# Kernel tuning notes

Hardware: AMD Instinct MI355X
Metric: run time of the kernel (lower is better)

## Reference

```python
import jax, jax.numpy as jnp
import numpy as np

C = 1024
H = 16
HS = C // H
HID = 4096
A_MIX = 0.7
B_MIX = 0.3
EPS = 1e-5


def layernorm(x, w, b):
    mu = jnp.mean(x, axis=-1, keepdims=True)
    var = jnp.mean(jnp.square(x - mu), axis=-1, keepdims=True)
    return (x - mu) * jax.lax.rsqrt(var + EPS) * w + b


def setup_inputs() -> dict:
    key = jax.random.key(0)
    ks = jax.random.split(key, 12)
    B, N = 4, 1024
    s = 1.0 / np.sqrt(C)
    sh = 1.0 / np.sqrt(HID)
    return {
        "x": jax.random.normal(ks[0], (B, N, C), jnp.float32),
        "Query": jax.random.normal(ks[1], (B, H, N, HS), jnp.float32),
        "Key": jax.random.normal(ks[2], (B, H, N, HS), jnp.float32),
        "Value": jax.random.normal(ks[3], (B, H, N, HS), jnp.float32),
        "ln_w": jnp.ones((C,), jnp.float32),
        "ln_b": jnp.zeros((C,), jnp.float32),
        "qk_w": jax.random.normal(ks[4], (2 * C, C), jnp.float32) * s,
        "qk_b": jnp.zeros((2 * C,), jnp.float32),
        "v_w": jax.random.normal(ks[5], (C, C), jnp.float32) * s,
        "v_b": jnp.zeros((C,), jnp.float32),
        "out_w": jax.random.normal(ks[6], (C, C), jnp.float32) * s,
        "out_b": jnp.zeros((C,), jnp.float32),
        "mlp_w1": jax.random.normal(ks[7], (HID, C), jnp.float32) * s,
        "mlp_b1": jnp.zeros((HID,), jnp.float32),
        "mlp_w2": jax.random.normal(ks[8], (C, HID), jnp.float32) * sh,
        "mlp_b2": jnp.zeros((C,), jnp.float32),
    }


def reference(x, Query, Key, Value, ln_w, ln_b, qk_w, qk_b, v_w, v_b,
              out_w, out_b, mlp_w1, mlp_b1, mlp_w2, mlp_b2):
    B, N, _ = x.shape
    x1 = x
    xn = layernorm(x, ln_w, ln_b)
    # qk projection -> view (B,N,H,HS,2), permute -> (2,B,H,N,HS)
    qk = (xn @ qk_w.T + qk_b).reshape(B, N, H, HS, 2)
    Q = jnp.transpose(qk[..., 0], (0, 2, 1, 3))  # (B,H,N,HS)
    K = jnp.transpose(qk[..., 1], (0, 2, 1, 3))
    V = jnp.transpose((xn @ v_w.T + v_b).reshape(B, N, H, HS), (0, 2, 1, 3))
    Query = A_MIX * Q + B_MIX * Query
    Key = A_MIX * K + B_MIX * Key
    Value = B_MIX * Value + A_MIX * V
    attn = jnp.einsum('bhqd,bhkd->bhqk', Query, Key) / np.sqrt(HS)
    attn = jax.nn.softmax(attn, axis=-1)  # dropout = identity in eval
    o = jnp.einsum('bhqk,bhkd->bhqd', attn, Value)
    o = jnp.transpose(o, (0, 2, 1, 3)).reshape(B, N, C)
    o = o @ out_w.T + out_b
    x = x1 + o
    x2 = x
    xn2 = layernorm(x, ln_w, ln_b)  # same layernorm params reused
    h = jax.nn.gelu(xn2 @ mlp_w1.T + mlp_b1, approximate=False)
    m = h @ mlp_w2.T + mlp_b2
    return (m + x2, Query, Key, Value)
```

## Files before the change

### kernel.cpp

```cpp
#include <hip/hip_runtime.h>

using bf16x8 = __attribute__((ext_vector_type(8))) __bf16;
using f32x4  = __attribute__((ext_vector_type(4))) float;

#define AS1(p) (const __attribute__((address_space(1))) void*)(p)
#define AS3(p) (__attribute__((address_space(3))) void*)(p)

__device__ __forceinline__ unsigned short f2bf(float f) {
    unsigned int u = __float_as_uint(f);
    unsigned int r = (u + 0x7FFFu + ((u >> 16) & 1u)) >> 16;
    return (unsigned short)r;
}
__device__ __forceinline__ float bf2f(unsigned short u) {
    return __uint_as_float((unsigned int)u << 16);
}
__device__ __forceinline__ float gelu_fast(float x) {
    const float a = 1.5957691f * (x + 0.044715f * x * x * x);
    return x / (1.0f + __expf(-a));
}

__global__ __launch_bounds__(256) void cvt_kernel(const float* __restrict__ in,
                                                  unsigned short* __restrict__ out,
                                                  int n) {
    int i = (blockIdx.x * 256 + threadIdx.x) * 4;
    if (i < n) {
        float4 v = *(const float4*)(in + i);
        ushort4 o = make_ushort4(f2bf(v.x), f2bf(v.y), f2bf(v.z), f2bf(v.w));
        *(ushort4*)(out + i) = o;
    }
}

__global__ __launch_bounds__(256) void ln_kernel(const float* __restrict__ in,
                                                 const float* __restrict__ w,
                                                 const float* __restrict__ b,
                                                 unsigned short* __restrict__ out) {
    const int row = blockIdx.x;
    const int tid = threadIdx.x;
    const float4 v = *(const float4*)(in + (size_t)row * 1024 + tid * 4);
    float s  = v.x + v.y + v.z + v.w;
    float ss = v.x * v.x + v.y * v.y + v.z * v.z + v.w * v.w;
    #pragma unroll
    for (int m = 1; m < 64; m <<= 1) {
        s  += __shfl_xor(s, m, 64);
        ss += __shfl_xor(ss, m, 64);
    }
    __shared__ float red[8];
    if ((tid & 63) == 0) { red[(tid >> 6) * 2] = s; red[(tid >> 6) * 2 + 1] = ss; }
    __syncthreads();
    s  = red[0] + red[2] + red[4] + red[6];
    ss = red[1] + red[3] + red[5] + red[7];
    const float mu  = s * (1.0f / 1024.0f);
    const float var = ss * (1.0f / 1024.0f) - mu * mu;
    const float rstd = rsqrtf(var + 1e-5f);
    const float4 wv = *(const float4*)(w + tid * 4);
    const float4 bv = *(const float4*)(b + tid * 4);
    ushort4 o;
    o.x = f2bf((v.x - mu) * rstd * wv.x + bv.x);
    o.y = f2bf((v.y - mu) * rstd * wv.y + bv.y);
    o.z = f2bf((v.z - mu) * rstd * wv.z + bv.z);
    o.w = f2bf((v.w - mu) * rstd * wv.w + bv.w);
    *(ushort4*)(out + (size_t)row * 1024 + tid * 4) = o;
}

template <int EPI>
__global__ __launch_bounds__(256, 2)
void gemm_bt(const unsigned short* __restrict__ A,
             const unsigned short* __restrict__ W,
             const float* __restrict__ bias,
             int M, int N, int K,
             const float* __restrict__ e0, const float* __restrict__ e1,
             float* __restrict__ o0, float* __restrict__ o1,
             unsigned short* __restrict__ u0, unsigned short* __restrict__ u1) {
    __shared__ unsigned short As[128 * 128];
    __shared__ unsigned short Bs[128 * 128];
    const int tid  = threadIdx.x;
    const int wave = tid >> 6, lane = tid & 63;
    const int wr = wave >> 1, wc = wave & 1;
    const int q15 = lane & 15, g = lane >> 4;

    const int gx = gridDim.x;
    const int nwg = gx * gridDim.y;
    int flat = blockIdx.y * gx + blockIdx.x;
    flat = (flat & 7) * (nwg >> 3) + (flat >> 3);
    const int gm0 = (flat / gx) * 128, gn0 = (flat % gx) * 128;

    f32x4 acc[4][4] = {};

    const int lrow4 = lane >> 4;
    const int lslot = lane & 15;
    const int rswz  = q15 << 4;

    for (int k0 = 0; k0 < K; k0 += 128) {
        #pragma unroll
        for (int i = 0; i < 8; ++i) {
            const int row  = wave * 32 + i * 4 + lrow4;
            const int selm = (lslot ^ (row & 15)) << 3;
            __builtin_amdgcn_global_load_lds(AS1(A + (size_t)(gm0 + row) * K + k0 + selm),
                                             AS3((char*)As + wave * 8192 + i * 1024), 16, 0, 0);
            __builtin_amdgcn_global_load_lds(AS1(W + (size_t)(gn0 + row) * K + k0 + selm),
                                             AS3((char*)Bs + wave * 8192 + i * 1024), 16, 0, 0);
        }
        __syncthreads();
        #pragma unroll
        for (int kk = 0; kk < 4; ++kk) {
            bf16x8 af[4], bfr[4];
            #pragma unroll
            for (int m = 0; m < 4; ++m)
                af[m] = *(const bf16x8*)((char*)As + (wr * 64 + m * 16 + q15) * 256 +
                                         ((kk * 64 + g * 16) ^ rswz));
            #pragma unroll
            for (int n = 0; n < 4; ++n)
                bfr[n] = *(const bf16x8*)((char*)Bs + (wc * 64 + n * 16 + q15) * 256 +
                                          ((kk * 64 + g * 16) ^ rswz));
            #pragma unroll
            for (int m = 0; m < 4; ++m)
                #pragma unroll
                for (int n = 0; n < 4; ++n)
                    acc[m][n] = __builtin_amdgcn_mfma_f32_16x16x32_bf16(af[m], bfr[n], acc[m][n], 0, 0, 0);
        }
        __syncthreads();
    }

    #pragma unroll
    for (int m = 0; m < 4; ++m)
    #pragma unroll
    for (int n = 0; n < 4; ++n)
    #pragma unroll
    for (int j = 0; j < 4; ++j) {
        const int r = gm0 + wr * 64 + m * 16 + g * 4 + j;
        const int c = gn0 + wc * 64 + n * 16 + q15;
        const float val = acc[m][n][j] + bias[c];
        if constexpr (EPI == 0) {
            const int bb = r >> 10, nn = r & 1023;
            const int h = c >> 7, hs = (c >> 1) & 63, isk = c & 1;
            const size_t idx = (((size_t)(bb * 16 + h)) * 1024 + nn) * 64 + hs;
            if (!isk) { const float mx = 0.7f * val + 0.3f * e0[idx]; o0[idx] = mx; u0[idx] = f2bf(mx); }
            else      { const float mx = 0.7f * val + 0.3f * e1[idx]; o1[idx] = mx; u1[idx] = f2bf(mx); }
        } else if constexpr (EPI == 1) {
            const int bb = r >> 10, nn = r & 1023;
            const int h = c >> 6, hs = c & 63;
            const size_t idx = (((size_t)(bb * 16 + h)) * 1024 + nn) * 64 + hs;
            const float mx = 0.7f * val + 0.3f * e0[idx];
            o0[idx] = mx;
            u0[(((size_t)(bb * 16 + h)) * 64 + hs) * 1024 + nn] = f2bf(mx);
        } else if constexpr (EPI == 2) {
            const size_t idx = (size_t)r * N + c;
            o0[idx] = val + e0[idx];
        } else {
            const size_t idx = (size_t)r * N + c;
            o0[idx] = val + e0[idx];
        }
    }
}

__global__ __launch_bounds__(512, 1)
void gemm_big_gelu(const unsigned short* __restrict__ A,
                   const unsigned short* __restrict__ W,
                   const float* __restrict__ bias,
                   int M, int N, int K,
                   unsigned short* __restrict__ u0) {
    __shared__ unsigned short As[256 * 64];
    __shared__ unsigned short Bs[256 * 64];
    const int tid  = threadIdx.x;
    const int wave = tid >> 6, lane = tid & 63;
    const int wr = wave >> 2, wc = wave & 3;
    const int q15 = lane & 15, g = lane >> 4;

    const int gx = gridDim.x;
    const int nwg = gx * gridDim.y;
    int flat = blockIdx.y * gx + blockIdx.x;
    flat = (flat & 7) * (nwg >> 3) + (flat >> 3);
    const int gm0 = (flat / gx) * 256, gn0 = (flat % gx) * 256;

    f32x4 acc[8][4] = {};

    const int srow8 = lane >> 3;
    const int selm  = (((lane & 7) ^ srow8) << 3);
    const int rswz  = (q15 & 7) << 4;

    for (int k0 = 0; k0 < K; k0 += 64) {
        #pragma unroll
        for (int i = 0; i < 4; ++i) {
            const int row = i * 64 + wave * 8 + srow8;
            __builtin_amdgcn_global_load_lds(AS1(A + (size_t)(gm0 + row) * K + k0 + selm),
                                             AS3((char*)As + (i * 64 + wave * 8) * 128), 16, 0, 0);
            __builtin_amdgcn_global_load_lds(AS1(W + (size_t)(gn0 + row) * K + k0 + selm),
                                             AS3((char*)Bs + (i * 64 + wave * 8) * 128), 16, 0, 0);
        }
        __syncthreads();
        #pragma unroll
        for (int kk = 0; kk < 2; ++kk) {
            bf16x8 af[8], bfr[4];
            #pragma unroll
            for (int m = 0; m < 8; ++m)
                af[m] = *(const bf16x8*)((char*)As + (wr * 128 + m * 16 + q15) * 128 +
                                         ((kk * 64 + g * 16) ^ rswz));
            #pragma unroll
            for (int n = 0; n < 4; ++n)
                bfr[n] = *(const bf16x8*)((char*)Bs + (wc * 64 + n * 16 + q15) * 128 +
                                          ((kk * 64 + g * 16) ^ rswz));
            #pragma unroll
            for (int m = 0; m < 8; ++m)
                #pragma unroll
                for (int n = 0; n < 4; ++n)
                    acc[m][n] = __builtin_amdgcn_mfma_f32_16x16x32_bf16(af[m], bfr[n], acc[m][n], 0, 0, 0);
        }
        __syncthreads();
    }

    #pragma unroll
    for (int m = 0; m < 8; ++m)
    #pragma unroll
    for (int n = 0; n < 4; ++n)
    #pragma unroll
    for (int j = 0; j < 4; ++j) {
        const int r = gm0 + wr * 128 + m * 16 + g * 4 + j;
        const int c = gn0 + wc * 64 + n * 16 + q15;
        const float val = acc[m][n][j] + bias[c];
        u0[(size_t)r * N + c] = f2bf(gelu_fast(val));
    }
}

__global__ __launch_bounds__(256, 6)
void attn_kernel(const unsigned short* __restrict__ Qb,
                 const unsigned short* __restrict__ Kb,
                 const unsigned short* __restrict__ Vt,
                 unsigned short* __restrict__ Op,
                 float* __restrict__ Mws,
                 float* __restrict__ Lws) {
    const int bh = blockIdx.y;
    const int z  = blockIdx.z;
    const int tid = threadIdx.x, wave = tid >> 6, lane = tid & 63;
    const int qbase = blockIdx.x * 64 + wave * 16;
    const int q15 = lane & 15, g = lane >> 4;

    const unsigned short* Qh = Qb + (size_t)bh * 1024 * 64;
    const unsigned short* Kh = Kb + (size_t)bh * 1024 * 64;
    const unsigned short* Vh = Vt + (size_t)bh * 64 * 1024;

    __shared__ alignas(128) unsigned short Ks[64 * 64];
    __shared__ alignas(128) unsigned short Vs[64 * 64];
    __shared__ alignas(128) unsigned short Ps[4][1024];
    char* const Pb = (char*)Ps[wave] + q15 * 128;
    const int swz = (q15 & 7) << 4;

    const int srow8 = lane >> 3;
    const int selm  = (((lane & 7) ^ srow8) << 3);

    bf16x8 aq[2];
    aq[0] = *(const bf16x8*)&Qh[(size_t)(qbase + q15) * 64 + 0  + g * 8];
    aq[1] = *(const bf16x8*)&Qh[(size_t)(qbase + q15) * 64 + 32 + g * 8];

    f32x4 o[4] = {};
    float mrow = -1e30f, lrow = 0.f;

    const int t0 = z * 8;
    for (int t = t0; t < t0 + 8; ++t) {
        const int kb = t * 64;
        #pragma unroll
        for (int i = 0; i < 2; ++i) {
            const int r = wave * 16 + i * 8 + srow8;
            __builtin_amdgcn_global_load_lds(AS1(Kh + (size_t)(kb + r) * 64 + selm),
                                             AS3((char*)Ks + wave * 2048 + i * 1024), 16, 0, 0);
            __builtin_amdgcn_global_load_lds(AS1(Vh + (size_t)r * 1024 + kb + selm),
                                             AS3((char*)Vs + wave * 2048 + i * 1024), 16, 0, 0);
        }
        __syncthreads();

        f32x4 s[4] = {};
        #pragma unroll
        for (int kt = 0; kt < 4; ++kt) {
            #pragma unroll
            for (int kk = 0; kk < 2; ++kk) {
                const bf16x8 bk = *(const bf16x8*)((char*)Ks + (kt * 16 + q15) * 128 +
                                                   ((kk * 64 + g * 16) ^ swz));
                s[kt] = __builtin_amdgcn_mfma_f32_16x16x32_bf16(bk, aq[kk], s[kt], 0, 0, 0);
            }
        }
        float pm = -1e30f;
        #pragma unroll
        for (int kt = 0; kt < 4; ++kt) {
            s[kt] *= 0.125f;
            pm = fmaxf(pm, fmaxf(fmaxf(s[kt][0], s[kt][1]), fmaxf(s[kt][2], s[kt][3])));
        }
        pm = fmaxf(pm, __shfl_xor(pm, 16, 64));
        pm = fmaxf(pm, __shfl_xor(pm, 32, 64));
        const float mnew = fmaxf(mrow, pm);
        const float alpha = __expf(mrow - mnew);
        mrow = mnew;

        float rs = 0.f;
        #pragma unroll
        for (int kt = 0; kt < 4; ++kt) {
            const float p0 = __expf(s[kt][0] - mnew);
            const float p1 = __expf(s[kt][1] - mnew);
            const float p2 = __expf(s[kt][2] - mnew);
            const float p3 = __expf(s[kt][3] - mnew);
            rs += (p0 + p1) + (p2 + p3);
            uint2 pk;
            pk.x = (unsigned int)f2bf(p0) | ((unsigned int)f2bf(p1) << 16);
            pk.y = (unsigned int)f2bf(p2) | ((unsigned int)f2bf(p3) << 16);
            *(uint2*)(Pb + (((kt * 32 + g * 8) ^ swz))) = pk;
        }
        rs += __shfl_xor(rs, 16, 64);
        rs += __shfl_xor(rs, 32, 64);
        lrow = lrow * alpha + rs;

        float af[4];
        #pragma unroll
        for (int j = 0; j < 4; ++j) af[j] = __shfl(alpha, g * 4 + j, 64);
        #pragma unroll
        for (int dt = 0; dt < 4; ++dt)
            #pragma unroll
            for (int j = 0; j < 4; ++j) o[dt][j] *= af[j];

        #pragma unroll
        for (int Bb = 0; Bb < 2; ++Bb) {
            const bf16x8 pa = *(const bf16x8*)(Pb + (((Bb * 64 + g * 16) ^ swz)));
            #pragma unroll
            for (int dt = 0; dt < 4; ++dt) {
                const bf16x8 vb = *(const bf16x8*)((char*)Vs + (dt * 16 + q15) * 128 +
                                                   ((Bb * 64 + g * 16) ^ swz));
                o[dt] = __builtin_amdgcn_mfma_f32_16x16x32_bf16(pa, vb, o[dt], 0, 0, 0);
            }
        }
        __syncthreads();
    }

    #pragma unroll
    for (int dt = 0; dt < 4; ++dt)
        #pragma unroll
        for (int j = 0; j < 4; ++j) {
            const int q = qbase + g * 4 + j;
            Op[(((size_t)z * 64 + bh) * 1024 + q) * 64 + dt * 16 + q15] = f2bf(o[dt][j]);
        }
    if (g == 0) {
        const size_t mi = ((size_t)z * 64 + bh) * 1024 + qbase + q15;
        Mws[mi] = mrow;
        Lws[mi] = lrow;
    }
}

__global__ __launch_bounds__(256)
void attn_combine(const unsigned short* __restrict__ Op,
                  const float* __restrict__ Mws,
                  const float* __restrict__ Lws,
                  unsigned short* __restrict__ Ob) {
    const int e4 = blockIdx.x * 256 + threadIdx.x;
    const int d0 = (e4 & 15) * 4;
    const int q  = (e4 >> 4) & 1023;
    const int bh = e4 >> 14;
    const size_t base0 = (((size_t)bh) * 1024 + q) * 64 + d0;
    const size_t base1 = (((size_t)(64 + bh)) * 1024 + q) * 64 + d0;
    const ushort4 a = *(const ushort4*)&Op[base0];
    const ushort4 c = *(const ushort4*)&Op[base1];
    const size_t mi0 = (size_t)bh * 1024 + q;
    const size_t mi1 = mi0 + 64 * 1024;
    const float m0 = Mws[mi0], m1 = Mws[mi1];
    const float l0 = Lws[mi0], l1 = Lws[mi1];
    const float m  = fmaxf(m0, m1);
    const float w0 = __expf(m0 - m), w1 = __expf(m1 - m);
    const float inv = 1.0f / (l0 * w0 + l1 * w1);
    ushort4 r;
    r.x = f2bf((bf2f(a.x) * w0 + bf2f(c.x) * w1) * inv);
    r.y = f2bf((bf2f(a.y) * w0 + bf2f(c.y) * w1) * inv);
    r.z = f2bf((bf2f(a.z) * w0 + bf2f(c.z) * w1) * inv);
    r.w = f2bf((bf2f(a.w) * w0 + bf2f(c.w) * w1) * inv);
    const int b = bh >> 4, h = bh & 15;
    *(ushort4*)&Ob[((size_t)(b * 1024 + q)) * 1024 + h * 64 + d0] = r;
}

extern "C" void kernel_launch(void* const* d_in, const int* in_sizes, int n_in,
                              void* d_out, int out_size, void* d_ws, size_t ws_size,
                              hipStream_t stream) {
    (void)in_sizes; (void)n_in; (void)out_size; (void)ws_size;
    const float* x     = (const float*)d_in[0];
    const float* Qin   = (const float*)d_in[1];
    const float* Kin   = (const float*)d_in[2];
    const float* Vin   = (const float*)d_in[3];
    const float* ln_w  = (const float*)d_in[4];
    const float* ln_b  = (const float*)d_in[5];
    const float* qk_w  = (const float*)d_in[6];
    const float* qk_b  = (const float*)d_in[7];
    const float* v_w   = (const float*)d_in[8];
    const float* v_b   = (const float*)d_in[9];
    const float* out_w = (const float*)d_in[10];
    const float* out_b = (const float*)d_in[11];
    const float* w1    = (const float*)d_in[12];
    const float* b1    = (const float*)d_in[13];
    const float* w2    = (const float*)d_in[14];
    const float* b2    = (const float*)d_in[15];

    const size_t FOUR_M = (size_t)4 * 1024 * 1024;
    float* out0 = (float*)d_out;
    float* Qout = out0 + FOUR_M;
    float* Kout = Qout + FOUR_M;
    float* Vout = Kout + FOUR_M;

    char* ws = (char*)d_ws;
    const size_t MB = 1024 * 1024;
    unsigned short* xn   = (unsigned short*)(ws + 0);
    unsigned short* qkwb = (unsigned short*)(ws + 8 * MB);
    unsigned short* vwb  = (unsigned short*)(ws + 12 * MB);
    unsigned short* owb  = (unsigned short*)(ws + 14 * MB);
    unsigned short* w1b  = (unsigned short*)(ws + 16 * MB);
    unsigned short* w2b  = (unsigned short*)(ws + 24 * MB);
    unsigned short* Qbuf = (unsigned short*)(ws + 32 * MB);
    unsigned short* Kbuf = (unsigned short*)(ws + 40 * MB);
    unsigned short* Vtb  = (unsigned short*)(ws + 48 * MB);
    unsigned short* atto = (unsigned short*)(ws + 56 * MB);
    unsigned short* hbuf = (unsigned short*)(ws + 32 * MB);
    float* y1 = (float*)(ws + 64 * MB);
    unsigned short* Oprt = (unsigned short*)(ws + 64 * MB);
    float* Mws = (float*)(ws + 8 * MB);
    float* Lws = (float*)(ws + 8 * MB + 512 * 1024);

    cvt_kernel<<<2048, 256, 0, stream>>>(qk_w, qkwb, 2048 * 1024);
    cvt_kernel<<<1024, 256, 0, stream>>>(v_w,  vwb,  1024 * 1024);
    cvt_kernel<<<1024, 256, 0, stream>>>(out_w, owb, 1024 * 1024);
    cvt_kernel<<<4096, 256, 0, stream>>>(w1, w1b, 4096 * 1024);
    cvt_kernel<<<4096, 256, 0, stream>>>(w2, w2b, 4096 * 1024);

    ln_kernel<<<4096, 256, 0, stream>>>(x, ln_w, ln_b, xn);

    {
        dim3 g(2048 / 128, 4096 / 128);
        gemm_bt<0><<<g, 256, 0, stream>>>(xn, qkwb, qk_b, 4096, 2048, 1024,
                                          Qin, Kin, Qout, Kout, Qbuf, Kbuf);
    }
    {
        dim3 g(1024 / 128, 4096 / 128);
        gemm_bt<1><<<g, 256, 0, stream>>>(xn, vwb, v_b, 4096, 1024, 1024,
                                          Vin, nullptr, Vout, nullptr, Vtb, nullptr);
    }
    {
        dim3 g(16, 64, 2);
        attn_kernel<<<g, 256, 0, stream>>>(Qbuf, Kbuf, Vtb, Oprt, Mws, Lws);
        attn_combine<<<4096, 256, 0, stream>>>(Oprt, Mws, Lws, atto);
    }
    {
        dim3 g(1024 / 128, 4096 / 128);
        gemm_bt<2><<<g, 256, 0, stream>>>(atto, owb, out_b, 4096, 1024, 1024,
                                          x, nullptr, y1, nullptr, nullptr, nullptr);
    }
    ln_kernel<<<4096, 256, 0, stream>>>(y1, ln_w, ln_b, xn);
    {
        dim3 g(4096 / 256, 4096 / 256);
        gemm_big_gelu<<<g, 512, 0, stream>>>(xn, w1b, b1, 4096, 4096, 1024, hbuf);
    }
    {
        dim3 g(1024 / 128, 4096 / 128);
        gemm_bt<4><<<g, 256, 0, stream>>>(hbuf, w2b, b2, 4096, 1024, 4096,
                                          y1, nullptr, out0, nullptr, nullptr, nullptr);
    }
}
```

Baseline: 266.9 us.

## Split-K the second MLP GEMM with 256x256 tiles and bf16 partial combine

```diff
diff --git a/kernel.cpp b/kernel.cpp
--- a/kernel.cpp
+++ b/kernel.cpp
@@ -143,9 +143,6 @@
             const float mx = 0.7f * val + 0.3f * e0[idx];
             o0[idx] = mx;
             u0[(((size_t)(bb * 16 + h)) * 64 + hs) * 1024 + nn] = f2bf(mx);
-        } else if constexpr (EPI == 2) {
-            const size_t idx = (size_t)r * N + c;
-            o0[idx] = val + e0[idx];
         } else {
             const size_t idx = (size_t)r * N + c;
             o0[idx] = val + e0[idx];
@@ -153,12 +150,15 @@
     }
 }
 
+template <int EPI>
 __global__ __launch_bounds__(512, 1)
-void gemm_big_gelu(const unsigned short* __restrict__ A,
-                   const unsigned short* __restrict__ W,
-                   const float* __restrict__ bias,
-                   int M, int N, int K,
-                   unsigned short* __restrict__ u0) {
+void gemm_big(const unsigned short* __restrict__ A,
+              const unsigned short* __restrict__ W,
+              const float* __restrict__ bias,
+              int M, int N, int lda, int Kc,
+              const float* __restrict__ e0,
+              float* __restrict__ o0,
+              unsigned short* __restrict__ u0) {
     __shared__ unsigned short As[256 * 64];
     __shared__ unsigned short Bs[256 * 64];
     const int tid  = threadIdx.x;
@@ -171,6 +171,7 @@
     int flat = blockIdx.y * gx + blockIdx.x;
     flat = (flat & 7) * (nwg >> 3) + (flat >> 3);
     const int gm0 = (flat / gx) * 256, gn0 = (flat % gx) * 256;
+    const int k0base = blockIdx.z * Kc;
 
     f32x4 acc[8][4] = {};
 
@@ -178,13 +179,13 @@
     const int selm  = (((lane & 7) ^ srow8) << 3);
     const int rswz  = (q15 & 7) << 4;
 
-    for (int k0 = 0; k0 < K; k0 += 64) {
+    for (int k0 = k0base; k0 < k0base + Kc; k0 += 64) {
         #pragma unroll
         for (int i = 0; i < 4; ++i) {
             const int row = i * 64 + wave * 8 + srow8;
-            __builtin_amdgcn_global_load_lds(AS1(A + (size_t)(gm0 + row) * K + k0 + selm),
+            __builtin_amdgcn_global_load_lds(AS1(A + (size_t)(gm0 + row) * lda + k0 + selm),
                                              AS3((char*)As + (i * 64 + wave * 8) * 128), 16, 0, 0);
-            __builtin_amdgcn_global_load_lds(AS1(W + (size_t)(gn0 + row) * K + k0 + selm),
+            __builtin_amdgcn_global_load_lds(AS1(W + (size_t)(gn0 + row) * lda + k0 + selm),
                                              AS3((char*)Bs + (i * 64 + wave * 8) * 128), 16, 0, 0);
         }
         __syncthreads();
@@ -216,8 +217,36 @@
     for (int j = 0; j < 4; ++j) {
         const int r = gm0 + wr * 128 + m * 16 + g * 4 + j;
         const int c = gn0 + wc * 64 + n * 16 + q15;
-        const float val = acc[m][n][j] + bias[c];
-        u0[(size_t)r * N + c] = f2bf(gelu_fast(val));
+        if constexpr (EPI == 0) {
+            const float val = acc[m][n][j] + bias[c];
+            u0[(size_t)r * N + c] = f2bf(gelu_fast(val));
+        } else {
+            if (blockIdx.z == 0) {
+                const float val = acc[m][n][j] + bias[c];
+                const size_t idx = (size_t)r * N + c;
+                o0[idx] = val + e0[idx];
+            } else {
+                u0[((size_t)(blockIdx.z - 1) * M + r) * N + c] = f2bf(acc[m][n][j]);
+            }
+        }
+    }
+}
+
+__global__ __launch_bounds__(256)
+void mlp2_combine(float* __restrict__ out0,
+                  const unsigned short* __restrict__ Pp,
+                  int total) {
+    const int i = (blockIdx.x * 256 + threadIdx.x) * 4;
+    if (i < total) {
+        float4 v = *(float4*)(out0 + i);
+        const ushort4 p1 = *(const ushort4*)&Pp[i];
+        const ushort4 p2 = *(const ushort4*)&Pp[(size_t)total + i];
+        const ushort4 p3 = *(const ushort4*)&Pp[(size_t)2 * total + i];
+        v.x += bf2f(p1.x) + bf2f(p2.x) + bf2f(p3.x);
+        v.y += bf2f(p1.y) + bf2f(p2.y) + bf2f(p3.y);
+        v.z += bf2f(p1.z) + bf2f(p2.z) + bf2f(p3.z);
+        v.w += bf2f(p1.w) + bf2f(p2.w) + bf2f(p3.w);
+        *(float4*)(out0 + i) = v;
     }
 }
 
@@ -414,6 +443,7 @@
     unsigned short* Oprt = (unsigned short*)(ws + 64 * MB);
     float* Mws = (float*)(ws + 8 * MB);
     float* Lws = (float*)(ws + 8 * MB + 512 * 1024);
+    unsigned short* Pmlp = (unsigned short*)(ws + 0);
 
     cvt_kernel<<<2048, 256, 0, stream>>>(qk_w, qkwb, 2048 * 1024);
     cvt_kernel<<<1024, 256, 0, stream>>>(v_w,  vwb,  1024 * 1024);
@@ -445,12 +475,14 @@
     }
     ln_kernel<<<4096, 256, 0, stream>>>(y1, ln_w, ln_b, xn);
     {
-        dim3 g(4096 / 256, 4096 / 256);
-        gemm_big_gelu<<<g, 512, 0, stream>>>(xn, w1b, b1, 4096, 4096, 1024, hbuf);
-    }
-    {
-        dim3 g(1024 / 128, 4096 / 128);
-        gemm_bt<4><<<g, 256, 0, stream>>>(hbuf, w2b, b2, 4096, 1024, 4096,
-                                          y1, nullptr, out0, nullptr, nullptr, nullptr);
-    }
-}
+        dim3 g(4096 / 256, 4096 / 256, 1);
+        gemm_big<0><<<g, 512, 0, stream>>>(xn, w1b, b1, 4096, 4096, 1024, 1024,
+                                           nullptr, nullptr, hbuf);
+    }
+    {
+        dim3 g(1024 / 256, 4096 / 256, 4);
+        gemm_big<1><<<g, 512, 0, stream>>>(hbuf, w2b, b2, 4096, 1024, 4096, 1024,
+                                           y1, out0, Pmlp);
+        mlp2_combine<<<4096, 256, 0, stream>>>(out0, Pmlp, 4 * 1024 * 1024);
+    }
+}
```

Result: slower. 293.7 us (+10.1%).

## Triple-buffer LDS in MLP up-projection GEMM with async prefetch two tiles ahead

Applied to the files above, without the earlier changes.

```diff
diff --git a/kernel.cpp b/kernel.cpp
--- a/kernel.cpp
+++ b/kernel.cpp
@@ -143,9 +143,6 @@
             const float mx = 0.7f * val + 0.3f * e0[idx];
             o0[idx] = mx;
             u0[(((size_t)(bb * 16 + h)) * 64 + hs) * 1024 + nn] = f2bf(mx);
-        } else if constexpr (EPI == 2) {
-            const size_t idx = (size_t)r * N + c;
-            o0[idx] = val + e0[idx];
         } else {
             const size_t idx = (size_t)r * N + c;
             o0[idx] = val + e0[idx];
@@ -159,8 +156,7 @@
                    const float* __restrict__ bias,
                    int M, int N, int K,
                    unsigned short* __restrict__ u0) {
-    __shared__ unsigned short As[256 * 64];
-    __shared__ unsigned short Bs[256 * 64];
+    __shared__ unsigned short Ls[3][2][256 * 32];
     const int tid  = threadIdx.x;
     const int wave = tid >> 6, lane = tid & 63;
     const int wr = wave >> 2, wc = wave & 3;
@@ -174,39 +170,62 @@
 
     f32x4 acc[8][4] = {};
 
-    const int srow8 = lane >> 3;
-    const int selm  = (((lane & 7) ^ srow8) << 3);
-    const int rswz  = (q15 & 7) << 4;
-
-    for (int k0 = 0; k0 < K; k0 += 64) {
-        #pragma unroll
-        for (int i = 0; i < 4; ++i) {
-            const int row = i * 64 + wave * 8 + srow8;
-            __builtin_amdgcn_global_load_lds(AS1(A + (size_t)(gm0 + row) * K + k0 + selm),
-                                             AS3((char*)As + (i * 64 + wave * 8) * 128), 16, 0, 0);
-            __builtin_amdgcn_global_load_lds(AS1(W + (size_t)(gn0 + row) * K + k0 + selm),
-                                             AS3((char*)Bs + (i * 64 + wave * 8) * 128), 16, 0, 0);
-        }
-        __syncthreads();
-        #pragma unroll
-        for (int kk = 0; kk < 2; ++kk) {
-            bf16x8 af[8], bfr[4];
-            #pragma unroll
-            for (int m = 0; m < 8; ++m)
-                af[m] = *(const bf16x8*)((char*)As + (wr * 128 + m * 16 + q15) * 128 +
-                                         ((kk * 64 + g * 16) ^ rswz));
-            #pragma unroll
-            for (int n = 0; n < 4; ++n)
-                bfr[n] = *(const bf16x8*)((char*)Bs + (wc * 64 + n * 16 + q15) * 128 +
-                                          ((kk * 64 + g * 16) ^ rswz));
-            #pragma unroll
-            for (int m = 0; m < 8; ++m)
+    const int srow  = tid >> 2;
+    const int sslot = (tid & 3) ^ ((srow >> 1) & 3);
+    const int selm  = sslot << 3;
+
+    #define STAGEH(kt, p, rb)                                                        \
+        {                                                                            \
+            const unsigned short* src_ = ((p) < 2) ? A : W;                          \
+            const int gbase_ = ((p) < 2) ? gm0 : gn0;                                \
+            const int row_ = ((p) & 1) * 128 + srow;                                 \
+            __builtin_amdgcn_global_load_lds(                                        \
+                AS1(src_ + (size_t)(gbase_ + row_) * K + (kt) * 32 + selm),          \
+                AS3((char*)Ls[rb][(p) >> 1] + ((p) & 1) * 8192 + tid * 16),          \
+                16, 0, 0);                                                           \
+        }
+
+    const int nt = K >> 5;
+    #pragma unroll
+    for (int p = 0; p < 4; ++p) STAGEH(0, p, 0);
+    #pragma unroll
+    for (int p = 0; p < 4; ++p) STAGEH(1, p, 1);
+
+    int rb = 0;
+    for (int t = 0; t < nt; ++t) {
+        if (t >= nt - 1) { asm volatile("s_waitcnt vmcnt(0)" ::: "memory"); }
+        else             { asm volatile("s_waitcnt vmcnt(4)" ::: "memory"); }
+        asm volatile("s_barrier" ::: "memory");
+        const int rb2 = (rb >= 1) ? rb - 1 : rb + 2;
+        const char* Ab = (const char*)Ls[rb][0];
+        const char* Bb = (const char*)Ls[rb][1];
+        #pragma unroll
+        for (int p = 0; p < 4; ++p) {
+            if (t + 2 < nt) STAGEH(t + 2, p, rb2);
+            const int mh = p >> 1, nh = p & 1;
+            bf16x8 af[4], bf[2];
+            #pragma unroll
+            for (int mm = 0; mm < 4; ++mm) {
+                const int row = wr * 128 + mh * 64 + mm * 16 + q15;
+                af[mm] = *(const bf16x8*)(Ab + row * 64 + ((g ^ ((row >> 1) & 3)) << 4));
+            }
+            #pragma unroll
+            for (int nn = 0; nn < 2; ++nn) {
+                const int row = wc * 64 + nh * 32 + nn * 16 + q15;
+                bf[nn] = *(const bf16x8*)(Bb + row * 64 + ((g ^ ((row >> 1) & 3)) << 4));
+            }
+            __builtin_amdgcn_s_setprio(1);
+            #pragma unroll
+            for (int mm = 0; mm < 4; ++mm)
                 #pragma unroll
-                for (int n = 0; n < 4; ++n)
-                    acc[m][n] = __builtin_amdgcn_mfma_f32_16x16x32_bf16(af[m], bfr[n], acc[m][n], 0, 0, 0);
-        }
-        __syncthreads();
-    }
+                for (int nn = 0; nn < 2; ++nn)
+                    acc[mh * 4 + mm][nh * 2 + nn] = __builtin_amdgcn_mfma_f32_16x16x32_bf16(
+                        af[mm], bf[nn], acc[mh * 4 + mm][nh * 2 + nn], 0, 0, 0);
+            __builtin_amdgcn_s_setprio(0);
+        }
+        rb = (rb == 2) ? 0 : rb + 1;
+    }
+    #undef STAGEH
 
     #pragma unroll
     for (int m = 0; m < 8; ++m)
@@ -450,7 +469,7 @@
     }
     {
         dim3 g(1024 / 128, 4096 / 128);
-        gemm_bt<4><<<g, 256, 0, stream>>>(hbuf, w2b, b2, 4096, 1024, 4096,
+        gemm_bt<2><<<g, 256, 0, stream>>>(hbuf, w2b, b2, 4096, 1024, 4096,
                                           y1, nullptr, out0, nullptr, nullptr, nullptr);
     }
 }
```

After: 259.8 us. 1.03x faster.
